# Optimization experiments

Measured on AMD Instinct MI355X. Metric: run time of the kernel, lower is better.

Reference implementation:

```python
import jax, jax.numpy as jnp
import numpy as np

NUM_HEADS = 8
SCALE = 25.0
SIM_THRESH = 0.75


def setup_inputs() -> dict:
    key = jax.random.key(0)
    ks = jax.random.split(key, 6)
    B, N, C = 1, 2048, 1024
    x_cls = jax.random.normal(ks[0], (B, N, C), jnp.float32)
    x_reg = jax.random.normal(ks[1], (B, N, C), jnp.float32)
    cls_score = jax.random.uniform(ks[2], (N,), jnp.float32)
    fg_score = jax.random.uniform(ks[3], (N,), jnp.float32)
    W_qkv_cls = jax.random.normal(ks[4], (3 * C, C), jnp.float32) * 0.02
    W_qkv_reg = jax.random.normal(ks[5], (3 * C, C), jnp.float32) * 0.02
    return {"x_cls": x_cls, "x_reg": x_reg, "cls_score": cls_score,
            "fg_score": fg_score, "W_qkv_cls": W_qkv_cls, "W_qkv_reg": W_qkv_reg}


def _l2norm(t):
    return t / jnp.linalg.norm(t, axis=-1, keepdims=True)


def reference(x_cls, x_reg, cls_score, fg_score, W_qkv_cls, W_qkv_reg):
    B, N, C = x_cls.shape
    H = NUM_HEADS
    d = C // H

    def qkv(x, W):
        # (B,N,3C) -> (3,B,H,N,d)
        t = (x @ W.T).reshape(B, N, 3, H, d).transpose(2, 0, 3, 1, 4)
        return t[0], t[1], t[2]

    q_cls, k_cls, v_cls = qkv(x_cls, W_qkv_cls)
    q_reg, k_reg, _ = qkv(x_reg, W_qkv_reg)

    q_cls, k_cls = _l2norm(q_cls), _l2norm(k_cls)
    q_reg, k_reg = _l2norm(q_reg), _l2norm(k_reg)
    v_cls_normed = _l2norm(v_cls)

    # scores broadcast: s[..., i, j] = score[j]; transpose -> score[i]
    s_cls = cls_score.reshape(1, 1, 1, N)
    s_fg = fg_score.reshape(1, 1, 1, N)
    # use_mask=True branch
    m_cls = (s_cls > jnp.swapaxes(s_cls, -2, -1) - 0.1).astype(x_cls.dtype)
    m_fg = (s_fg > jnp.swapaxes(s_fg, -2, -1) - 0.1).astype(x_cls.dtype)

    attn_cls_raw = jnp.einsum('bhid,bhjd->bhij', v_cls_normed, v_cls_normed)

    attn_cls = jax.nn.softmax(
        jnp.einsum('bhid,bhjd->bhij', q_cls, k_cls) * SCALE * s_cls * m_cls, axis=-1)
    attn_reg = jax.nn.softmax(
        jnp.einsum('bhid,bhjd->bhij', q_reg, k_reg) * SCALE * s_fg * m_fg, axis=-1)
    attn = (attn_reg + attn_cls) * 0.5

    x = jnp.einsum('bhij,bhjd->bhid', attn, v_cls).transpose(0, 2, 1, 3).reshape(B, N, C)
    x_ori = v_cls.transpose(0, 2, 1, 3).reshape(B, N, C)
    x_out = jnp.concatenate([x, x_ori], axis=-1)  # (B, N, 2C)

    # ave=True branch (batch 0, head-mean)
    raw = attn_cls_raw.sum(axis=1)[0] / H  # (N, N)
    sim_mask = (raw > SIM_THRESH).astype(x_cls.dtype)
    sim_attn = attn.sum(axis=1)[0] / H
    sim_round2 = jax.nn.softmax(sim_attn, axis=-1)
    sim_round2 = sim_mask * sim_round2
    sim_round2 = sim_round2 / jnp.sum(sim_round2, axis=-1, keepdims=True)
    return x_out, sim_round2
```

## Files before the change

kernel.cpp:

```cpp
#include <hip/hip_runtime.h>


#define NTOK 2048
#define CDIM 1024

typedef __attribute__((ext_vector_type(8))) short bf16x8;
typedef __attribute__((ext_vector_type(4))) short s16x4;
typedef __attribute__((ext_vector_type(2))) short s16x2;
typedef __attribute__((ext_vector_type(4))) float f32x4;

#define MFMA16(a,b,c) __builtin_amdgcn_mfma_f32_16x16x32_bf16((a),(b),(c),0,0,0)

__device__ __forceinline__ short f2bf(float x){
  unsigned u = __float_as_uint(x);
  u += 0x7FFFu + ((u >> 16) & 1u);
  return (short)(u >> 16);
}

__device__ __forceinline__ float bf2f(short s){
  return __uint_as_float(((unsigned)(unsigned short)s) << 16);
}

__device__ __forceinline__ int cvtpk(float lo, float hi){
  int r;
  asm("v_cvt_pk_bf16_f32 %0, %1, %2" : "=v"(r) : "v"(lo), "v"(hi));
  return r;
}

__device__ __forceinline__ void atomAddF(float* p, float v){
  unsafeAtomicAdd(p, v);
}

__device__ __forceinline__ void gld16(const short* g, short* l){
  __builtin_amdgcn_global_load_lds(
      (const __attribute__((address_space(1))) unsigned int*)g,
      (__attribute__((address_space(3))) unsigned int*)l, 16, 0, 0);
}

__global__ __launch_bounds__(256,8) void k_cvt(
    const float* __restrict__ xc, const float* __restrict__ xr,
    const float* __restrict__ Wc, const float* __restrict__ Wr,
    short* __restrict__ xbc, short* __restrict__ xbr,
    short* __restrict__ wbc, short* __restrict__ wbr)
{
  int idx = blockIdx.x*256 + threadIdx.x;
  const float* src; short* dst; int off;
  if      (idx <  262144){ src = xc; dst = xbc; off = idx; }
  else if (idx <  524288){ src = xr; dst = xbr; off = idx - 262144; }
  else if (idx <  917504){ src = Wc; dst = wbc; off = idx - 524288; }
  else                   { src = Wr; dst = wbr; off = idx - 917504; }
  float4 a = *(const float4*)(src + (size_t)off*8);
  float4 b = *(const float4*)(src + (size_t)off*8 + 4);
  bf16x8 o = { f2bf(a.x), f2bf(a.y), f2bf(a.z), f2bf(a.w),
               f2bf(b.x), f2bf(b.y), f2bf(b.z), f2bf(b.w) };
  *(bf16x8*)(dst + (size_t)off*8) = o;
}

__global__ __launch_bounds__(256,3) void k_qkv(
    const short* __restrict__ xbc, const short* __restrict__ xbr,
    const short* __restrict__ wbc, const short* __restrict__ wbr,
    short* __restrict__ qc, short* __restrict__ kc,
    short* __restrict__ qr, short* __restrict__ kr,
    short* __restrict__ vn, short* __restrict__ vb,
    float* __restrict__ out)
{
  const int tid = threadIdx.x;
  const int l   = tid & 63;
  const int w   = tid >> 6;
  const int fr  = l & 15;
  const int g   = l >> 4;
  const int fk8 = g * 8;

  const int L     = blockIdx.x;
  const int xcd   = L & 7;
  const int slot  = L >> 3;
  const int panel = xcd*5 + (slot >> 4);
  const int mb    = slot & 15;
  const int m0    = mb * 128;
  const int o0    = panel * 128;

  const short* Xb; const short* Wb; int wrow;
  if (o0 < 3072){ Xb = xbc; Wb = wbc; wrow = o0; }
  else          { Xb = xbr; Wb = wbr; wrow = o0 - 3072; }

  __shared__ __align__(16) short Ab[2][8][64][8];
  __shared__ __align__(16) short Bb[2][8][64][8];
  __shared__ float nbuf[128][2];

  const int wr = w >> 1;
  const int wc = w & 1;

#define QSTAGE(DB, KN) do {                                                  \
    _Pragma("unroll")                                                        \
    for (int it=0; it<2; ++it){                                              \
      int f = it*4 + w;                                                      \
      gld16(Xb + (size_t)(m0  + f*16 + fr)*CDIM + (KN) + fk8,                \
            &Ab[DB][f][0][0]);                                               \
      gld16(Wb + (size_t)(wrow + f*16 + fr)*CDIM + (KN) + fk8,               \
            &Bb[DB][f][0][0]);                                               \
    }                                                                        \
  } while(0)

  f32x4 acc[4][4] = {};

  QSTAGE(0, 0);
  __syncthreads();

  for (int kt = 0; kt < 32; ++kt){
    const int db = kt & 1;
    if (kt < 31){ if (db) QSTAGE(0, (kt+1)*32); else QSTAGE(1, (kt+1)*32); }
    bf16x8 af[4], bfr[4];
    #pragma unroll
    for (int ai=0;ai<4;ai++) af[ai]  = *(const bf16x8*)&Ab[db][wr*4+ai][l][0];
    #pragma unroll
    for (int bj=0;bj<4;bj++) bfr[bj] = *(const bf16x8*)&Bb[db][wc*4+bj][l][0];
    #pragma unroll
    for (int ai=0;ai<4;ai++)
      #pragma unroll
      for (int bj=0;bj<4;bj++)
        acc[ai][bj] = MFMA16(af[ai], bfr[bj], acc[ai][bj]);
    __syncthreads();
  }
#undef QSTAGE

  const int chunk = o0 >> 10;
  const int hh    = (o0 >> 7) & 7;

  float rn[4][4];
  #pragma unroll
  for (int ai=0;ai<4;ai++)
    #pragma unroll
    for (int r=0;r<4;r++){
      float ss = 0.f;
      #pragma unroll
      for (int bj=0;bj<4;bj++) ss += acc[ai][bj][r]*acc[ai][bj][r];
      ss += __shfl_xor(ss, 1); ss += __shfl_xor(ss, 2);
      ss += __shfl_xor(ss, 4); ss += __shfl_xor(ss, 8);
      if (fr == 0) nbuf[wr*64 + ai*16 + g*4 + r][wc] = ss;
      rn[ai][r] = ss;
    }
  __syncthreads();
  #pragma unroll
  for (int ai=0;ai<4;ai++)
    #pragma unroll
    for (int r=0;r<4;r++){
      int row = wr*64 + ai*16 + g*4 + r;
      rn[ai][r] = rsqrtf(nbuf[row][0] + nbuf[row][1]);
    }

  #pragma unroll
  for (int ai=0;ai<4;ai++)
    #pragma unroll
    for (int r=0;r<4;r++){
      int n   = m0 + wr*64 + ai*16 + g*4 + r;
      size_t base = ((size_t)hh*NTOK + n)*128;
      #pragma unroll
      for (int bj=0;bj<4;bj++){
        int col = wc*64 + bj*16 + fr;
        float val = acc[ai][bj][r];
        short nv  = f2bf(val * rn[ai][r]);
        switch(chunk){
          case 0: qc[base+col] = nv; break;
          case 1: kc[base+col] = nv; break;
          case 3: qr[base+col] = nv; break;
          case 4: kr[base+col] = nv; break;
          default:
            vn[base+col] = nv;
            vb[base+col] = f2bf(val);
            out[(size_t)n*2048 + 1024 + hh*128 + col] = val;
            break;
        }
      }
    }
}

__global__ __launch_bounds__(256,4) void k_vT(
    const short* __restrict__ vb, short* __restrict__ vT)
{
  int b = blockIdx.x;
  int h  = b >> 6;
  int nt = (b >> 1) & 31;
  int dt = b & 1;
  __shared__ short t[64][72];
  int tid = threadIdx.x;
  int r  = tid >> 2;
  int c0 = (tid & 3) << 4;
  #pragma unroll
  for (int u=0;u<2;u++){
    bf16x8 val = *(const bf16x8*)&vb[((size_t)h*NTOK + nt*64 + r)*128 + dt*64 + c0 + u*8];
    #pragma unroll
    for (int e=0;e<8;e++) t[r][c0+u*8+e] = val[e];
  }
  __syncthreads();
  #pragma unroll
  for (int u=0;u<2;u++){
    bf16x8 o;
    #pragma unroll
    for (int e=0;e<8;e++) o[e] = t[c0+u*8+e][r];
    *(bf16x8*)&vT[((size_t)h*128 + dt*64 + r)*NTOK + nt*64 + c0 + u*8] = o;
  }
}

#define JLEN 1024

__global__ __launch_bounds__(512,4) void k_attn(
    const short* __restrict__ qc, const short* __restrict__ kc,
    const short* __restrict__ qr, const short* __restrict__ kr,
    const short* __restrict__ vT,
    const float* __restrict__ csc, const float* __restrict__ fsc,
    float* __restrict__ s_cls, float* __restrict__ s_reg,
    short* __restrict__ Up)
{
  const int tid = threadIdx.x;
  const int l   = tid & 63;
  const int w   = tid >> 6;
  const int L    = blockIdx.x;
  const int xcd  = L & 7;
  const int slot = L >> 3;
  const int hs   = ((slot >> 5) << 3) | xcd;
  const int h    = hs >> 1;
  const int s    = hs & 1;
  const int rem  = slot & 31;
  const int js   = rem >> 4;
  const int ib   = rem & 15;

  const int iw  = ib * 128 + w * 16;
  const int fr  = l & 15;
  const int g   = l >> 4;
  const int fk8 = g * 8;
  const size_t hN = (size_t)h * NTOK;
  const size_t hD = (size_t)h * 128;

  const short* Qp = s ? qr : qc;
  const short* Kp = s ? kr : kc;
  const float* sc = s ? fsc : csc;
  float* ssum     = s ? s_reg : s_cls;
  short* Ub       = Up + (size_t)(js*2 + s) * 2097152;

  __shared__ __align__(16) short Kbuf[2][4][4][64][8];
  __shared__ __align__(16) short Vbuf[2][8][2][64][8];

  const int t4 = w * 4;

#define STAGE(DB, JN) do {                                                   \
    _Pragma("unroll")                                                        \
    for (int q4=0; q4<4; ++q4){                                              \
      int t = t4 + q4;                                                       \
      if (t < 16){                                                           \
        int jf = t >> 2, kk = t & 3;                                         \
        gld16(Kp + (hN + (JN) + jf*16 + fr)*128 + kk*32 + fk8,               \
              &Kbuf[DB][jf][kk][0][0]);                                      \
      } else {                                                               \
        int u = t - 16, df = u >> 1, ks = u & 1;                             \
        gld16(vT + (hD + df*16 + fr)*2048 + (JN) + ks*32 + fk8,              \
              &Vbuf[DB][df][ks][0][0]);                                      \
      }                                                                      \
    }                                                                        \
  } while(0)

  bf16x8 bq[4];
  #pragma unroll
  for (int kk=0;kk<4;kk++)
    bq[kk] = *(const bf16x8*)&Qp[(hN + iw + fr)*128 + kk*32 + fk8];

  const float sci = sc[iw + fr] - 0.1f;

  f32x4 U[8] = {};
  float p = 0.f;

  const int srcA = ((((g<<1)    & 3) << 4) + fr) << 2;
  const int srcB = ((((g<<1 | 1)& 3) << 4) + fr) << 2;
  const bool ghi = g >= 2;
  const int jbase = js * JLEN;

  STAGE(0, jbase);
  __syncthreads();

  for (int jt = 0; jt < 16; ++jt){
    const int db = jt & 1;
    const int j0 = jbase + jt*64;
    if (jt < 15){ if (db) STAGE(0, j0 + 64); else STAGE(1, j0 + 64); }
    #pragma unroll
    for (int ks=0; ks<2; ++ks){
      int cpk[2][2];
      #pragma unroll
      for (int t=0; t<2; ++t){
        const int jf = ks*2 + t;
        f32x4 S0 = {};
        __builtin_amdgcn_s_setprio(1);
        #pragma unroll
        for (int kk=0; kk<4; ++kk){
          bf16x8 kb = *(const bf16x8*)&Kbuf[db][jf][kk][l][0];
          S0 = MFMA16(kb, bq[kk], S0);
        }
        __builtin_amdgcn_s_setprio(0);
        float4 sjv = *(const float4*)&sc[j0 + jf*16 + 4*g];
        float e0[4];
        #pragma unroll
        for (int r=0;r<4;r++){
          float sj = (&sjv.x)[r];
          float sj25 = 25.0f * sj;
          e0[r] = (sj > sci) ? __expf(S0[r]*sj25) : 1.0f;
          p += e0[r];
        }
        cpk[t][0] = cvtpk(e0[0], e0[1]);
        cpk[t][1] = cvtpk(e0[2], e0[3]);
      }
      int a0 = __builtin_amdgcn_ds_bpermute(srcA, cpk[0][0]);
      int a1 = __builtin_amdgcn_ds_bpermute(srcA, cpk[0][1]);
      int a2 = __builtin_amdgcn_ds_bpermute(srcA, cpk[1][0]);
      int a3 = __builtin_amdgcn_ds_bpermute(srcA, cpk[1][1]);
      int b0 = __builtin_amdgcn_ds_bpermute(srcB, cpk[0][0]);
      int b1 = __builtin_amdgcn_ds_bpermute(srcB, cpk[0][1]);
      int b2 = __builtin_amdgcn_ds_bpermute(srcB, cpk[1][0]);
      int b3 = __builtin_amdgcn_ds_bpermute(srcB, cpk[1][1]);
      int wd[4];
      wd[0] = ghi ? a2 : a0;  wd[1] = ghi ? a3 : a1;
      wd[2] = ghi ? b2 : b0;  wd[3] = ghi ? b3 : b1;
      bf16x8 ea = *(bf16x8*)wd;
      __builtin_amdgcn_s_setprio(1);
      #pragma unroll
      for (int df=0; df<8; ++df){
        bf16x8 bv = *(const bf16x8*)&Vbuf[db][df][ks][l][0];
        U[df] = MFMA16(ea, bv, U[df]);
      }
      __builtin_amdgcn_s_setprio(0);
    }
    __syncthreads();
  }
#undef STAGE

  p += __shfl_xor(p, 16);
  p += __shfl_xor(p, 32);
  if (l < 16)
    atomAddF(&ssum[hN + iw + l], p);
  #pragma unroll
  for (int df=0;df<8;df++)
    #pragma unroll
    for (int r=0;r<4;r++)
      Ub[(hN + iw + g*4 + r)*128 + df*16 + fr] = f2bf(U[df][r]);
}

__global__ __launch_bounds__(256,8) void k_attn_fin(
    const short* __restrict__ Up,
    const float* __restrict__ s_cls, const float* __restrict__ s_reg,
    float* __restrict__ out)
{
  int task = blockIdx.x*4 + (threadIdx.x>>6);
  int lane = threadIdx.x & 63;
  int h = task >> 11;
  int row = task & 2047;
  size_t b = (size_t)task*128 + lane*2;
  float cx=0.f, cy=0.f, rx=0.f, ry=0.f;
  #pragma unroll
  for (int js=0; js<2; ++js){
    s16x2 c = *(const s16x2*)(Up + (size_t)(js*2+0)*2097152 + b);
    s16x2 r = *(const s16x2*)(Up + (size_t)(js*2+1)*2097152 + b);
    cx += bf2f(c[0]); cy += bf2f(c[1]);
    rx += bf2f(r[0]); ry += bf2f(r[1]);
  }
  float isc = 0.5f/s_cls[task];
  float isr = 0.5f/s_reg[task];
  float2 o = { cx*isc + rx*isr, cy*isc + ry*isr };
  *(float2*)&out[(size_t)row*2048 + h*128 + lane*2] = o;
}

__global__ __launch_bounds__(256,2) void k_sim(
    const short* __restrict__ qc, const short* __restrict__ kc,
    const short* __restrict__ qr, const short* __restrict__ kr,
    const short* __restrict__ vn,
    const float* __restrict__ csc, const float* __restrict__ fsc,
    const float* __restrict__ s_cls, const float* __restrict__ s_reg,
    unsigned char* __restrict__ mask, float* __restrict__ out)
{
  const int tid  = threadIdx.x;
  const int lane = tid & 63;
  const int w    = tid >> 6;
  const int i0w  = blockIdx.x * 128 + w * 32;
  const int j0   = blockIdx.y * 64;
  const int fr   = lane & 15;
  const int fk   = (lane >> 4) * 8;

  __shared__ __align__(16) short Bsh[3][16][64][8];

  float sjc[4], sjf[4];
  #pragma unroll
  for (int js=0;js<4;js++){ sjc[js]=csc[j0+js*16+fr]; sjf[js]=fsc[j0+js*16+fr]; }
  int rowb[2]; float sci[2][4], sfi[2][4];
  #pragma unroll
  for (int ri=0;ri<2;ri++){
    rowb[ri] = i0w + ri*16 + ((lane>>4)<<2);
    #pragma unroll
    for (int r=0;r<4;r++){ sci[ri][r]=csc[rowb[ri]+r]; sfi[ri][r]=fsc[rowb[ri]+r]; }
  }

  f32x4 sim[2][4] = {};
  f32x4 raw[2][4] = {};

  for (int h=0; h<8; ++h){
    const size_t hb = (size_t)h * NTOK;
    bf16x8 aq[2][4], ar[2][4], av[2][4];
    #pragma unroll
    for (int ri=0;ri<2;ri++)
      #pragma unroll
      for (int kk=0;kk<4;kk++){
        aq[ri][kk] = *(const bf16x8*)&qc[(hb + i0w + ri*16 + fr)*128 + kk*32 + fk];
        ar[ri][kk] = *(const bf16x8*)&qr[(hb + i0w + ri*16 + fr)*128 + kk*32 + fk];
        av[ri][kk] = *(const bf16x8*)&vn[(hb + i0w + ri*16 + fr)*128 + kk*32 + fk];
      }
    float iscl[2][4], isrl[2][4];
    #pragma unroll
    for (int ri=0;ri<2;ri++)
      #pragma unroll
      for (int r=0;r<4;r++){
        iscl[ri][r] = 1.0f/s_cls[hb + rowb[ri] + r];
        isrl[ri][r] = 1.0f/s_reg[hb + rowb[ri] + r];
      }
    __syncthreads();
    #pragma unroll
    for (int it=0; it<12; ++it){
      int slot = it*256 + tid;
      int str  = slot >> 10;
      int frag = (slot >> 6) & 15;
      int l    = slot & 63;
      int r    = (frag >> 2)*16 + (l & 15);
      int c    = (frag & 3)*32 + (l >> 4)*8;
      const short* gp = (str==0 ? kc : (str==1 ? kr : vn)) + (hb + j0 + r)*128 + c;
      *(bf16x8*)&Bsh[str][frag][l][0] = *(const bf16x8*)gp;
    }
    __syncthreads();
    #pragma unroll
    for (int js=0; js<4; ++js){
      bf16x8 bc[4], br[4], bv[4];
      #pragma unroll
      for (int kk=0;kk<4;kk++){
        bc[kk] = *(const bf16x8*)&Bsh[0][js*4+kk][lane][0];
        br[kk] = *(const bf16x8*)&Bsh[1][js*4+kk][lane][0];
        bv[kk] = *(const bf16x8*)&Bsh[2][js*4+kk][lane][0];
      }
      #pragma unroll
      for (int ri=0;ri<2;ri++){
        f32x4 Sc = {}; f32x4 Sr = {};
        #pragma unroll
        for (int kk=0;kk<4;kk++){
          Sc = MFMA16(aq[ri][kk], bc[kk], Sc);
          Sr = MFMA16(ar[ri][kk], br[kk], Sr);
          raw[ri][js] = MFMA16(av[ri][kk], bv[kk], raw[ri][js]);
        }
        #pragma unroll
        for (int r=0;r<4;r++){
          float ec = (sjc[js] > sci[ri][r]-0.1f) ? __expf(Sc[r]*(25.0f*sjc[js])) : 1.0f;
          float er = (sjf[js] > sfi[ri][r]-0.1f) ? __expf(Sr[r]*(25.0f*sjf[js])) : 1.0f;
          sim[ri][js][r] += ec*iscl[ri][r] + er*isrl[ri][r];
        }
      }
    }
  }
  #pragma unroll
  for (int ri=0;ri<2;ri++)
    #pragma unroll
    for (int js=0;js<4;js++)
      #pragma unroll
      for (int r=0;r<4;r++){
        int orow = rowb[ri] + r;
        int ocol = j0 + js*16 + fr;
        out[4194304ull + (size_t)orow*2048 + ocol] = sim[ri][js][r] * 0.0625f;
        mask[(size_t)orow*2048 + ocol] = raw[ri][js][r] > 6.0f ? 1 : 0;
      }
}

__global__ __launch_bounds__(256,4) void k_final(
    float* __restrict__ out, const unsigned char* __restrict__ mask)
{
  int row  = blockIdx.x*4 + (threadIdx.x>>6);
  int lane = threadIdx.x & 63;
  float* sr = out + 4194304ull + (size_t)row*2048;
  const unsigned char* mr = mask + (size_t)row*2048;
  float v[32];
  float sum2 = 0.0f;
  #pragma unroll
  for (int c=0;c<32;c++){
    float e = __expf(sr[c*64 + lane]);
    v[c] = (mr[c*64 + lane] != 0) ? e : 0.0f;
    sum2 += v[c];
  }
  #pragma unroll
  for (int m=1;m<64;m<<=1) sum2 += __shfl_xor(sum2, m);
  float inv = 1.0f / sum2;
  #pragma unroll
  for (int c=0;c<32;c++) sr[c*64 + lane] = v[c]*inv;
}

extern "C" void kernel_launch(void* const* d_in, const int* in_sizes, int n_in,
                              void* d_out, int out_size, void* d_ws, size_t ws_size,
                              hipStream_t stream)
{
  const float* xcls = (const float*)d_in[0];
  const float* xreg = (const float*)d_in[1];
  const float* csc  = (const float*)d_in[2];
  const float* fsc  = (const float*)d_in[3];
  const float* Wc   = (const float*)d_in[4];
  const float* Wr   = (const float*)d_in[5];
  float* out = (float*)d_out;

  char* ws = (char*)d_ws;
  short* xbc = (short*)ws;
  short* xbr = xbc + 2097152;
  short* wbc = xbr + 2097152;
  short* wbr = wbc + 3145728;
  unsigned char* mask = (unsigned char*)ws;
  char* accbase       = ws + 4u*1024*1024;
  float* s_cls        = (float*)(accbase);
  float* s_reg        = (float*)(accbase + 65536);
  short* Up           = (short*)(accbase + 131072);
  short* qc = (short*)(ws + 41943040ull);
  short* kc = qc + 2097152;
  short* qr = kc + 2097152;
  short* kr = qr + 2097152;
  short* vn = kr + 2097152;
  short* vb = vn + 2097152;
  short* vT = vb + 2097152;

  k_cvt  <<<4608,        256, 0, stream>>>(xcls, xreg, Wc, Wr, xbc, xbr, wbc, wbr);
  k_qkv  <<<640,         256, 0, stream>>>(xbc, xbr, wbc, wbr,
                                           qc, kc, qr, kr, vn, vb, out);
  k_vT   <<<512,         256, 0, stream>>>(vb, vT);
  hipMemsetAsync(accbase, 0, 131072, stream);
  k_attn <<<512,         512, 0, stream>>>(qc, kc, qr, kr, vT, csc, fsc,
                                           s_cls, s_reg, Up);
  k_attn_fin <<<4096,    256, 0, stream>>>(Up, s_cls, s_reg, out);
  k_sim  <<<dim3(16,32), 256, 0, stream>>>(qc, kc, qr, kr, vn, csc, fsc,
                                           s_cls, s_reg, mask, out);
  k_final<<<512,         256, 0, stream>>>(out, mask);
}
```

Before: 255.1 us.

## Double-buffer k_sim K/V tiles with async loads, halve tile width, remap blocks per XCD

Rewrites the k_sim similarity kernel. Each block now covers 32 columns instead of 64, and the grid becomes 1024 blocks in 1D, mapped so that blocks on the same XCD share column tiles. The per-head K/V tiles are staged into a double-buffered shared array with gld16 direct-to-LDS loads, prefetching head h+1 while head h computes, which replaces the two-barrier load-then-compute loop. It also raises the MFMA issue priority around the matmuls and targets three blocks per CU. Narrower tiles mean the per-row Q/R/V fragments are reloaded by twice as many blocks.

```diff
diff --git a/kernel.cpp b/kernel.cpp
--- a/kernel.cpp
+++ b/kernel.cpp
@@ -365,7 +365,7 @@
   *(float2*)&out[(size_t)row*2048 + h*128 + lane*2] = o;
 }
 
-__global__ __launch_bounds__(256,2) void k_sim(
+__global__ __launch_bounds__(256,3) void k_sim(
     const short* __restrict__ qc, const short* __restrict__ kc,
     const short* __restrict__ qr, const short* __restrict__ kr,
     const short* __restrict__ vn,
@@ -376,16 +376,21 @@
   const int tid  = threadIdx.x;
   const int lane = tid & 63;
   const int w    = tid >> 6;
-  const int i0w  = blockIdx.x * 128 + w * 32;
-  const int j0   = blockIdx.y * 64;
+  const int L    = blockIdx.x;
+  const int xcd  = L & 7;
+  const int slot = L >> 3;
+  const int yt   = xcd*8 + (slot >> 4);
+  const int xt   = slot & 15;
+  const int i0w  = xt*128 + w*32;
+  const int j0   = yt*32;
   const int fr   = lane & 15;
   const int fk   = (lane >> 4) * 8;
 
-  __shared__ __align__(16) short Bsh[3][16][64][8];
-
-  float sjc[4], sjf[4];
-  #pragma unroll
-  for (int js=0;js<4;js++){ sjc[js]=csc[j0+js*16+fr]; sjf[js]=fsc[j0+js*16+fr]; }
+  __shared__ __align__(16) short Bsh[2][3][8][64][8];
+
+  float sjc[2], sjf[2];
+  #pragma unroll
+  for (int js=0;js<2;js++){ sjc[js]=csc[j0+js*16+fr]; sjf[js]=fsc[j0+js*16+fr]; }
   int rowb[2]; float sci[2][4], sfi[2][4];
   #pragma unroll
   for (int ri=0;ri<2;ri++){
@@ -394,10 +399,29 @@
     for (int r=0;r<4;r++){ sci[ri][r]=csc[rowb[ri]+r]; sfi[ri][r]=fsc[rowb[ri]+r]; }
   }
 
-  f32x4 sim[2][4] = {};
-  f32x4 raw[2][4] = {};
+  f32x4 sim[2][2] = {};
+  f32x4 raw[2][2] = {};
+
+  const int t6 = w * 6;
+
+#define SSTAGE(DB, H) do {                                                   \
+    _Pragma("unroll")                                                        \
+    for (int q=0; q<6; ++q){                                                 \
+      int t   = t6 + q;                                           \
+      int str = t >> 3;                                  \
+      int f   = t & 7;                                          \
+      const short* gp = (str==0 ? kc : (str==1 ? kr : vn));                  \
+      gld16(gp + ((size_t)(H)*NTOK + j0 + (f>>2)*16 + fr)*128 + (f&3)*32 + fk,\
+            &Bsh[DB][str][f][0][0]);                                         \
+    }                                                                        \
+  } while(0)
+
+  SSTAGE(0, 0);
+  __syncthreads();
 
   for (int h=0; h<8; ++h){
+    const int db = h & 1;
+    if (h < 7){ if (db) SSTAGE(0, h+1); else SSTAGE(1, h+1); }
     const size_t hb = (size_t)h * NTOK;
     bf16x8 aq[2][4], ar[2][4], av[2][4];
     #pragma unroll
@@ -416,37 +440,26 @@
         iscl[ri][r] = 1.0f/s_cls[hb + rowb[ri] + r];
         isrl[ri][r] = 1.0f/s_reg[hb + rowb[ri] + r];
       }
-    __syncthreads();
-    #pragma unroll
-    for (int it=0; it<12; ++it){
-      int slot = it*256 + tid;
-      int str  = slot >> 10;
-      int frag = (slot >> 6) & 15;
-      int l    = slot & 63;
-      int r    = (frag >> 2)*16 + (l & 15);
-      int c    = (frag & 3)*32 + (l >> 4)*8;
-      const short* gp = (str==0 ? kc : (str==1 ? kr : vn)) + (hb + j0 + r)*128 + c;
-      *(bf16x8*)&Bsh[str][frag][l][0] = *(const bf16x8*)gp;
-    }
-    __syncthreads();
-    #pragma unroll
-    for (int js=0; js<4; ++js){
+    #pragma unroll
+    for (int js=0; js<2; ++js){
       bf16x8 bc[4], br[4], bv[4];
       #pragma unroll
       for (int kk=0;kk<4;kk++){
-        bc[kk] = *(const bf16x8*)&Bsh[0][js*4+kk][lane][0];
-        br[kk] = *(const bf16x8*)&Bsh[1][js*4+kk][lane][0];
-        bv[kk] = *(const bf16x8*)&Bsh[2][js*4+kk][lane][0];
+        bc[kk] = *(const bf16x8*)&Bsh[db][0][js*4+kk][lane][0];
+        br[kk] = *(const bf16x8*)&Bsh[db][1][js*4+kk][lane][0];
+        bv[kk] = *(const bf16x8*)&Bsh[db][2][js*4+kk][lane][0];
       }
       #pragma unroll
       for (int ri=0;ri<2;ri++){
         f32x4 Sc = {}; f32x4 Sr = {};
+        __builtin_amdgcn_s_setprio(1);
         #pragma unroll
         for (int kk=0;kk<4;kk++){
           Sc = MFMA16(aq[ri][kk], bc[kk], Sc);
           Sr = MFMA16(ar[ri][kk], br[kk], Sr);
           raw[ri][js] = MFMA16(av[ri][kk], bv[kk], raw[ri][js]);
         }
+        __builtin_amdgcn_s_setprio(0);
         #pragma unroll
         for (int r=0;r<4;r++){
           float ec = (sjc[js] > sci[ri][r]-0.1f) ? __expf(Sc[r]*(25.0f*sjc[js])) : 1.0f;
@@ -455,11 +468,14 @@
         }
       }
     }
-  }
+    __syncthreads();
+  }
+#undef SSTAGE
+
   #pragma unroll
   for (int ri=0;ri<2;ri++)
     #pragma unroll
-    for (int js=0;js<4;js++)
+    for (int js=0;js<2;js++)
       #pragma unroll
       for (int r=0;r<4;r++){
         int orow = rowb[ri] + r;
@@ -529,7 +545,7 @@
   k_attn <<<512,         512, 0, stream>>>(qc, kc, qr, kr, vT, csc, fsc,
                                            s_cls, s_reg, Up);
   k_attn_fin <<<4096,    256, 0, stream>>>(Up, s_cls, s_reg, out);
-  k_sim  <<<dim3(16,32), 256, 0, stream>>>(qc, kc, qr, kr, vn, csc, fsc,
+  k_sim  <<<1024,        256, 0, stream>>>(qc, kc, qr, kr, vn, csc, fsc,
                                            s_cls, s_reg, mask, out);
   k_final<<<512,         256, 0, stream>>>(out, mask);
 }
```

Result: slower. 464.6 us (+82.2%).
